# Optimization experiments

Hardware: AMD Instinct MI355X
Metric: run time of the kernel (lower is better)

## Reference

```python
import jax, jax.numpy as jnp
import numpy as np

DIM = 384
HEADS = 12
WIN = (7, 7)
N = WIN[0] * WIN[1]  # 49 tokens per window
B = 2048             # total windows
NW = 64              # windows per image (mask groups)


def _relative_position_index():
    ch, cw = np.meshgrid(np.arange(WIN[0]), np.arange(WIN[1]), indexing='ij')
    coords = np.stack([ch, cw]).reshape(2, -1)                 # [2, N]
    rel = coords[:, :, None] - coords[:, None, :]              # [2, N, N]
    rel = rel.transpose(1, 2, 0)                               # [N, N, 2]
    rel[..., 0] += WIN[0] - 1
    rel[..., 1] += WIN[1] - 1
    rel[..., 0] *= 2 * WIN[1] - 1
    return rel.sum(-1).astype(np.int32)                        # [N, N]


def setup_inputs() -> dict:
    key = jax.random.key(0)
    ks = jax.random.split(key, 7)
    table_sz = (2 * WIN[0] - 1) * (2 * WIN[1] - 1)             # 169
    return {
        'x': jax.random.normal(ks[0], (B, N, DIM), jnp.float32),
        'mask': jax.random.normal(ks[1], (NW, N, N), jnp.float32),
        'qkv_w': jax.random.normal(ks[2], (3 * DIM, DIM), jnp.float32) * (DIM ** -0.5),
        'qkv_b': jnp.zeros((3 * DIM,), jnp.float32),
        'proj_w': jax.random.normal(ks[3], (DIM, DIM), jnp.float32) * (DIM ** -0.5),
        'proj_b': jnp.zeros((DIM,), jnp.float32),
        'rel_table': jax.random.normal(ks[4], (table_sz, HEADS), jnp.float32) * 0.02,
        'rel_index': jnp.asarray(_relative_position_index()),
    }


def reference(x, mask, qkv_w, qkv_b, proj_w, proj_b, rel_table, rel_index):
    b, n, c = x.shape
    h, hd = HEADS, c // HEADS
    scale = hd ** -0.5
    qkv = (x @ qkv_w.T + qkv_b).reshape(b, n, 3, h, hd)
    q, k, v = (qkv[:, :, 0].transpose(0, 2, 1, 3),
               qkv[:, :, 1].transpose(0, 2, 1, 3),
               qkv[:, :, 2].transpose(0, 2, 1, 3))             # [b, h, n, hd]
    attn = jnp.einsum('bhid,bhjd->bhij', q * scale, k)         # [b, h, n, n]
    bias = rel_table[rel_index.reshape(-1)].reshape(n, n, h).transpose(2, 0, 1)
    attn = attn + bias[None]
    nw = mask.shape[0]
    attn = attn.reshape(b // nw, nw, h, n, n) + mask[None, :, None]
    attn = jax.nn.softmax(attn.reshape(b, h, n, n), axis=-1)
    out = jnp.einsum('bhij,bhjd->bihd', attn, v).reshape(b, n, c)
    return out @ proj_w.T + proj_b
```

## Files before the change

kernel.cpp:

```cpp
#include <hip/hip_runtime.h>

#define DIM   384
#define HEADS 12
#define NTOK  49
#define NWIN  2048
#define NMASK 64
#define HD    32
#define MTOT  (NWIN * NTOK)

typedef __bf16 bf16x8 __attribute__((ext_vector_type(8)));
typedef float  floatx4 __attribute__((ext_vector_type(4)));

__device__ __forceinline__ unsigned short f2bf(float f) {
  unsigned int u = __builtin_bit_cast(unsigned int, f);
  u += 0x7fffu + ((u >> 16) & 1u);
  return (unsigned short)(u >> 16);
}
__device__ __forceinline__ void async_copy16(const void* g, void* l) {
  __builtin_amdgcn_global_load_lds((const __attribute__((address_space(1))) void*)g,
                                   (__attribute__((address_space(3))) void*)l, 16, 0, 0);
}

__global__ void prep_kernel(const float* __restrict__ x,
                            const float* __restrict__ qkv_w,
                            const float* __restrict__ proj_w,
                            const float* __restrict__ rel_table,
                            const int*   __restrict__ rel_index,
                            unsigned short* __restrict__ xb,
                            unsigned short* __restrict__ qkv_wb,
                            unsigned short* __restrict__ proj_wb,
                            float* __restrict__ biasP) {
  const int tid  = blockIdx.x * blockDim.x + threadIdx.x;
  const int nthr = gridDim.x * blockDim.x;

  const int nx4 = (MTOT * DIM) / 4;
  for (int i = tid; i < nx4; i += nthr) {
    float4 v = ((const float4*)x)[i];
    ushort4 o = { f2bf(v.x), f2bf(v.y), f2bf(v.z), f2bf(v.w) };
    ((ushort4*)xb)[i] = o;
  }
  const int nw4 = (3 * DIM * DIM) / 4;
  for (int i = tid; i < nw4; i += nthr) {
    float4 v = ((const float4*)qkv_w)[i];
    ushort4 o = { f2bf(v.x), f2bf(v.y), f2bf(v.z), f2bf(v.w) };
    ((ushort4*)qkv_wb)[i] = o;
  }
  const int np4 = (DIM * DIM) / 4;
  for (int i = tid; i < np4; i += nthr) {
    float4 v = ((const float4*)proj_w)[i];
    ushort4 o = { f2bf(v.x), f2bf(v.y), f2bf(v.z), f2bf(v.w) };
    ((ushort4*)proj_wb)[i] = o;
  }
  for (int i = tid; i < 12288; i += nthr) {
    const int lane = i & 63;
    const int t    = (i >> 6) & 15;
    const int h    = i >> 10;
    const int rb   = (t >> 2) * 16 + (lane >> 4) * 4;
    const int c    = (t & 3) * 16 + (lane & 15);
    float4 o;
    float* op = (float*)&o;
#pragma unroll
    for (int reg = 0; reg < 4; reg++) {
      const int r = rb + reg;
      op[reg] = (r < NTOK && c < NTOK)
                  ? rel_table[rel_index[r * NTOK + c] * HEADS + h]
                  : -1e30f;
    }
    ((float4*)biasP)[i] = o;
  }
}

template <int OUT_BF16>
__global__ __launch_bounds__(256, 2)
void gemm_bt(const unsigned short* __restrict__ A,
             const unsigned short* __restrict__ W,
             const float* __restrict__ bias,
             void* __restrict__ Cout,
             int M, int N, int K) {
  constexpr int ESTR = OUT_BF16 ? 144 : 272;
  constexpr int ESZ  = 16 * ESTR;
  __shared__ __align__(16) char lds[OUT_BF16 ? (4 * 2 * 16 * 144)
                                             : (4 * 2 * 16 * 272)];
  char* ldsA = lds;
  char* ldsB = lds + 8192;

  const int tid  = threadIdx.x;
  const int lane = tid & 63;
  const int wave = tid >> 6;
  const int wr   = wave >> 1;
  const int wc   = wave & 1;
  const int q4   = lane >> 4;
  const int lm   = lane & 15;

  const int NT  = N >> 7;
  const int cpx = gridDim.x >> 3;
  const int lin = (blockIdx.x & 7) * cpx + (blockIdx.x >> 3);
  const int tileM = (lin / NT) * 128;
  const int tileN = (lin % NT) * 128;

  const int srow = tid >> 2;
  const int scol = (tid & 3) * 8;
  const unsigned short* gA = A + (size_t)(tileM + srow) * K + scol;
  const unsigned short* gB = W + (size_t)(tileN + srow) * K + scol;
  const int loff = tid * 16;

  const int aoff = (wr * 64 + lm) * 64 + q4 * 16;
  const int boff = (wc * 64 + lm) * 64 + q4 * 16;

  floatx4 acc[4][4] = {};

  for (int k0 = 0; k0 < K; k0 += 32) {
    async_copy16(gA,          ldsA + loff);
    async_copy16(gA + 64 * K, ldsA + 4096 + loff);
    async_copy16(gB,          ldsB + loff);
    async_copy16(gB + 64 * K, ldsB + 4096 + loff);
    gA += 32; gB += 32;
    __syncthreads();

    bf16x8 af[4], bfr[4];
#pragma unroll
    for (int i = 0; i < 4; i++) {
      af[i]  = *(const bf16x8*)(ldsA + aoff + i * 1024);
      bfr[i] = *(const bf16x8*)(ldsB + boff + i * 1024);
    }
#pragma unroll
    for (int i = 0; i < 4; i++)
#pragma unroll
      for (int j = 0; j < 4; j++)
        acc[i][j] = __builtin_amdgcn_mfma_f32_16x16x32_bf16(af[i], bfr[j], acc[i][j], 0, 0, 0);
    __syncthreads();
  }

  float bvj[4];
#pragma unroll
  for (int j = 0; j < 4; j++) bvj[j] = bias[tileN + wc * 64 + j * 16 + lm];

  char* Eb = lds + wave * (2 * ESZ);
#pragma unroll
  for (int i = 0; i < 4; i++) {
    char* Ep = Eb + (i & 1) * ESZ;
    if (OUT_BF16) {
#pragma unroll
      for (int j = 0; j < 4; j++)
#pragma unroll
        for (int r = 0; r < 4; r++)
          *(unsigned short*)(Ep + (q4 * 4 + r) * 144 + (j * 16 + lm) * 2) =
              f2bf(acc[i][j][r] + bvj[j]);
#pragma unroll
      for (int it = 0; it < 2; it++) {
        const int c   = lane + it * 64;
        const int row = c >> 3;
        const int c8  = c & 7;
        const uint4 v = *(const uint4*)(Ep + row * 144 + c8 * 16);
        unsigned short* dst = (unsigned short*)Cout +
            (size_t)(tileM + wr * 64 + i * 16 + row) * N + tileN + wc * 64 + c8 * 8;
        *(uint4*)dst = v;
      }
    } else {
#pragma unroll
      for (int j = 0; j < 4; j++)
#pragma unroll
        for (int r = 0; r < 4; r++)
          *(float*)(Ep + (q4 * 4 + r) * 272 + (j * 16 + lm) * 4) =
              acc[i][j][r] + bvj[j];
#pragma unroll
      for (int it = 0; it < 4; it++) {
        const int c   = lane + it * 64;
        const int row = c >> 4;
        const int c4  = c & 15;
        const uint4 v = *(const uint4*)(Ep + row * 272 + c4 * 16);
        float* dst = (float*)Cout +
            (size_t)(tileM + wr * 64 + i * 16 + row) * N + tileN + wc * 64 + c4 * 4;
        *(uint4*)dst = v;
      }
    }
  }
}

__global__ __launch_bounds__(256)
void attn_mfma(const unsigned short* __restrict__ qkv,
               const float* __restrict__ mask,
               const float* __restrict__ biasP,
               unsigned short* __restrict__ attn_out) {
  __shared__ __align__(16) char lds[4][16128];

  const int tid  = threadIdx.x;
  const int wave = tid >> 6;
  const int lane = tid & 63;
  const int lm   = lane & 15;
  const int q    = lane >> 4;

  const int pair = blockIdx.x * 4 + wave;
  const int b    = pair / HEADS;
  const int h    = pair - b * HEADS;
  const int g    = b & (NMASK - 1);

  char* Wl = lds[wave];
  char* Vt = Wl;
  char* Qb = Wl + 6912;
  char* Kb = Wl + 11008;
  char* Pb = Wl + 6912;

  const unsigned short* qbase = qkv + (size_t)b * NTOK * (3 * DIM) + h * HD;

  const uint4 zero16 = {0u, 0u, 0u, 0u};
#pragma unroll
  for (int r = 0; r < 4; r++) {
    const int row   = r * 16 + (lane >> 2);
    const int chunk = lane & 3;
    uint4 vq = zero16, vk = zero16;
    if (row < NTOK) {
      vq = *(const uint4*)(qbase + (size_t)row * (3 * DIM) + chunk * 8);
      vk = *(const uint4*)(qbase + (size_t)row * (3 * DIM) + DIM + chunk * 8);
    }
    *(uint4*)(Qb + row * 64 + chunk * 16) = vq;
    *(uint4*)(Kb + row * 64 + chunk * 16) = vk;
  }
  const unsigned short* vbase = qbase + 2 * DIM;
#pragma unroll 8
  for (int d = 0; d < HD; d++) {
    unsigned short v = 0;
    if (lane < NTOK) v = vbase[(size_t)lane * (3 * DIM) + d];
    *(unsigned short*)(Vt + d * 144 + lane * 2) = v;
  }
  *(unsigned short*)(Vt + HD * 144 + lane * 2) =
      (lane < NTOK) ? (unsigned short)0x3F80 : (unsigned short)0;

  bf16x8 qf[4], kf[4];
#pragma unroll
  for (int i = 0; i < 4; i++) {
    qf[i] = *(const bf16x8*)(Qb + (i * 16 + lm) * 64 + q * 16);
    kf[i] = *(const bf16x8*)(Kb + (i * 16 + lm) * 64 + q * 16);
  }
  floatx4 S[4][4] = {};
#pragma unroll
  for (int i = 0; i < 4; i++)
#pragma unroll
    for (int j = 0; j < 4; j++)
      S[i][j] = __builtin_amdgcn_mfma_f32_16x16x32_bf16(qf[i], kf[j], S[i][j], 0, 0, 0);

  const float scale = 0.17677669529663687f;
  const float*  bb  = biasP + (size_t)h * 4096;
  const float*  mb  = mask + (size_t)g * (NTOK * NTOK);
#pragma unroll
  for (int i = 0; i < 4; i++) {
#pragma unroll
    for (int j = 0; j < 4; j++) {
      const float4 bm4 = ((const float4*)bb)[(i * 4 + j) * 64 + lane];
      const float* bmp = (const float*)&bm4;
      const int cc = min(j * 16 + lm, NTOK - 1);
#pragma unroll
      for (int r = 0; r < 4; r++) {
        const int rr = min(i * 16 + q * 4 + r, NTOK - 1);
        const float mv = mb[rr * NTOK + cc];
        const float s  = fmaf(S[i][j][r], scale, bmp[r] + mv);
        const float p  = __expf(s);
        *(unsigned short*)(Pb + (i * 16 + q * 4 + r) * 144 + (j * 16 + lm) * 2) = f2bf(p);
      }
    }
  }

  floatx4 O[4][3] = {};
#pragma unroll
  for (int ks = 0; ks < 2; ks++) {
    bf16x8 pf[4], vf[3];
#pragma unroll
    for (int i = 0; i < 4; i++)
      pf[i] = *(const bf16x8*)(Pb + (i * 16 + lm) * 144 + ks * 64 + q * 16);
#pragma unroll
    for (int n = 0; n < 3; n++)
      vf[n] = *(const bf16x8*)(Vt + (n * 16 + lm) * 144 + ks * 64 + q * 16);
#pragma unroll
    for (int i = 0; i < 4; i++)
#pragma unroll
      for (int n = 0; n < 3; n++)
        O[i][n] = __builtin_amdgcn_mfma_f32_16x16x32_bf16(pf[i], vf[n], O[i][n], 0, 0, 0);
  }

  unsigned short* obase = attn_out + (size_t)b * NTOK * DIM + h * HD;
#pragma unroll
  for (int i = 0; i < 4; i++) {
#pragma unroll
    for (int r = 0; r < 4; r++) {
      const float sv  = __shfl(O[i][2][r], tid & 48, 64);
      const float inv = __builtin_amdgcn_rcpf(sv);
      const int row = i * 16 + q * 4 + r;
      if (row < NTOK) {
#pragma unroll
        for (int n = 0; n < 2; n++)
          obase[(size_t)row * DIM + n * 16 + lm] = f2bf(O[i][n][r] * inv);
      }
    }
  }
}

extern "C" void kernel_launch(void* const* d_in, const int* in_sizes, int n_in,
                              void* d_out, int out_size, void* d_ws, size_t ws_size,
                              hipStream_t stream) {
  const float* x         = (const float*)d_in[0];
  const float* mask      = (const float*)d_in[1];
  const float* qkv_w     = (const float*)d_in[2];
  const float* qkv_b     = (const float*)d_in[3];
  const float* proj_w    = (const float*)d_in[4];
  const float* proj_b    = (const float*)d_in[5];
  const float* rel_table = (const float*)d_in[6];
  const int*   rel_index = (const int*)d_in[7];
  float* out = (float*)d_out;

  char* ws = (char*)d_ws;
  unsigned short* xb      = (unsigned short*)(ws);
  unsigned short* qkvbuf  = (unsigned short*)(ws + 77070336);
  unsigned short* qkv_wb  = (unsigned short*)(ws + 308281344);
  unsigned short* proj_wb = (unsigned short*)(ws + 309166080);
  float*          biasP   = (float*)(ws + 309460992);

  prep_kernel<<<2048, 256, 0, stream>>>(x, qkv_w, proj_w, rel_table, rel_index,
                                        xb, qkv_wb, proj_wb, biasP);

  gemm_bt<1><<<dim3((MTOT / 128) * ((3 * DIM) / 128)), 256, 0, stream>>>(
      xb, qkv_wb, qkv_b, qkvbuf, MTOT, 3 * DIM, DIM);

  attn_mfma<<<dim3(NWIN * HEADS / 4), 256, 0, stream>>>(qkvbuf, mask, biasP,
                                                        xb );

  gemm_bt<0><<<dim3((MTOT / 128) * (DIM / 128)), 256, 0, stream>>>(
      xb , proj_wb, proj_b, out, MTOT, DIM, DIM);
}
```

Baseline: 608.9 us.

## Split attention per window-head across four waves and pre-pad mask into MFMA layout

The attention kernel now gives each 256-thread block a single (window, head) pair. Each of the four waves handles one 16-row query tile, sharing Q/K/V staged cooperatively in LDS behind __syncthreads, instead of one wave doing a whole pair alone. V transpose loading is vectorized, and the mask is pre-laid out in the prep kernel into padded MFMA fragment order so the softmax reads coalesced float4s. The block index is also remapped to spread consecutive blocks across the grid. This adds block barriers, 4x more blocks, and extra prep work and workspace for the padded mask.

```diff
diff --git a/kernel.cpp b/kernel.cpp
--- a/kernel.cpp
+++ b/kernel.cpp
@@ -26,10 +26,12 @@
                             const float* __restrict__ proj_w,
                             const float* __restrict__ rel_table,
                             const int*   __restrict__ rel_index,
+                            const float* __restrict__ mask,
                             unsigned short* __restrict__ xb,
                             unsigned short* __restrict__ qkv_wb,
                             unsigned short* __restrict__ proj_wb,
-                            float* __restrict__ biasP) {
+                            float* __restrict__ biasP,
+                            float* __restrict__ maskP) {
   const int tid  = blockIdx.x * blockDim.x + threadIdx.x;
   const int nthr = gridDim.x * blockDim.x;
 
@@ -67,6 +69,23 @@
                   : -1e30f;
     }
     ((float4*)biasP)[i] = o;
+  }
+  for (int i = tid; i < 65536; i += nthr) {
+    const int lane = i & 63;
+    const int t    = (i >> 6) & 15;
+    const int g    = i >> 10;
+    const int rb   = (t >> 2) * 16 + (lane >> 4) * 4;
+    const int c    = (t & 3) * 16 + (lane & 15);
+    float4 o;
+    float* op = (float*)&o;
+#pragma unroll
+    for (int reg = 0; reg < 4; reg++) {
+      const int r = rb + reg;
+      op[reg] = (r < NTOK && c < NTOK)
+                  ? mask[g * (NTOK * NTOK) + r * NTOK + c]
+                  : -1e30f;
+    }
+    ((float4*)maskP)[i] = o;
   }
 }
 
@@ -177,12 +196,16 @@
   }
 }
 
-__global__ __launch_bounds__(256)
+__global__ __launch_bounds__(256, 8)
 void attn_mfma(const unsigned short* __restrict__ qkv,
-               const float* __restrict__ mask,
                const float* __restrict__ biasP,
+               const float* __restrict__ maskP,
                unsigned short* __restrict__ attn_out) {
-  __shared__ __align__(16) char lds[4][16128];
+  __shared__ __align__(16) char lds[16128];
+  char* Vt = lds;
+  char* Qb = lds + 6912;
+  char* Kb = lds + 11008;
+  char* Pb = lds + 6912;
 
   const int tid  = threadIdx.x;
   const int wave = tid >> 6;
@@ -190,25 +213,17 @@
   const int lm   = lane & 15;
   const int q    = lane >> 4;
 
-  const int pair = blockIdx.x * 4 + wave;
+  const int pair = (blockIdx.x & 7) * (NWIN * HEADS / 8) + (blockIdx.x >> 3);
   const int b    = pair / HEADS;
   const int h    = pair - b * HEADS;
   const int g    = b & (NMASK - 1);
 
-  char* Wl = lds[wave];
-  char* Vt = Wl;
-  char* Qb = Wl + 6912;
-  char* Kb = Wl + 11008;
-  char* Pb = Wl + 6912;
-
   const unsigned short* qbase = qkv + (size_t)b * NTOK * (3 * DIM) + h * HD;
 
-  const uint4 zero16 = {0u, 0u, 0u, 0u};
-#pragma unroll
-  for (int r = 0; r < 4; r++) {
-    const int row   = r * 16 + (lane >> 2);
-    const int chunk = lane & 3;
-    uint4 vq = zero16, vk = zero16;
+  {
+    const int row   = tid >> 2;
+    const int chunk = tid & 3;
+    uint4 vq = {0u, 0u, 0u, 0u}, vk = vq;
     if (row < NTOK) {
       vq = *(const uint4*)(qbase + (size_t)row * (3 * DIM) + chunk * 8);
       vk = *(const uint4*)(qbase + (size_t)row * (3 * DIM) + DIM + chunk * 8);
@@ -216,80 +231,72 @@
     *(uint4*)(Qb + row * 64 + chunk * 16) = vq;
     *(uint4*)(Kb + row * 64 + chunk * 16) = vk;
   }
-  const unsigned short* vbase = qbase + 2 * DIM;
-#pragma unroll 8
-  for (int d = 0; d < HD; d++) {
-    unsigned short v = 0;
-    if (lane < NTOK) v = vbase[(size_t)lane * (3 * DIM) + d];
-    *(unsigned short*)(Vt + d * 144 + lane * 2) = v;
-  }
-  *(unsigned short*)(Vt + HD * 144 + lane * 2) =
-      (lane < NTOK) ? (unsigned short)0x3F80 : (unsigned short)0;
-
-  bf16x8 qf[4], kf[4];
-#pragma unroll
-  for (int i = 0; i < 4; i++) {
-    qf[i] = *(const bf16x8*)(Qb + (i * 16 + lm) * 64 + q * 16);
-    kf[i] = *(const bf16x8*)(Kb + (i * 16 + lm) * 64 + q * 16);
-  }
-  floatx4 S[4][4] = {};
-#pragma unroll
-  for (int i = 0; i < 4; i++)
-#pragma unroll
-    for (int j = 0; j < 4; j++)
-      S[i][j] = __builtin_amdgcn_mfma_f32_16x16x32_bf16(qf[i], kf[j], S[i][j], 0, 0, 0);
+  {
+    const int tok = tid >> 2;
+    const int c   = tid & 3;
+    uint4 vv = {0u, 0u, 0u, 0u};
+    if (tok < NTOK) vv = *(const uint4*)(qbase + 2 * DIM + (size_t)tok * (3 * DIM) + c * 8);
+    const unsigned short* e = (const unsigned short*)&vv;
+#pragma unroll
+    for (int j = 0; j < 8; j++)
+      *(unsigned short*)(Vt + (c * 8 + j) * 144 + tok * 2) = e[j];
+    if (tid < 64)
+      *(unsigned short*)(Vt + HD * 144 + tid * 2) =
+          (tid < NTOK) ? (unsigned short)0x3F80 : (unsigned short)0;
+  }
+  __syncthreads();
+
+  bf16x8 qf, kf[4];
+  qf = *(const bf16x8*)(Qb + (wave * 16 + lm) * 64 + q * 16);
+#pragma unroll
+  for (int j = 0; j < 4; j++)
+    kf[j] = *(const bf16x8*)(Kb + (j * 16 + lm) * 64 + q * 16);
+  floatx4 S[4] = {};
+#pragma unroll
+  for (int j = 0; j < 4; j++)
+    S[j] = __builtin_amdgcn_mfma_f32_16x16x32_bf16(qf, kf[j], S[j], 0, 0, 0);
+
+  __syncthreads();
 
   const float scale = 0.17677669529663687f;
-  const float*  bb  = biasP + (size_t)h * 4096;
-  const float*  mb  = mask + (size_t)g * (NTOK * NTOK);
-#pragma unroll
-  for (int i = 0; i < 4; i++) {
-#pragma unroll
-    for (int j = 0; j < 4; j++) {
-      const float4 bm4 = ((const float4*)bb)[(i * 4 + j) * 64 + lane];
-      const float* bmp = (const float*)&bm4;
-      const int cc = min(j * 16 + lm, NTOK - 1);
-#pragma unroll
-      for (int r = 0; r < 4; r++) {
-        const int rr = min(i * 16 + q * 4 + r, NTOK - 1);
-        const float mv = mb[rr * NTOK + cc];
-        const float s  = fmaf(S[i][j][r], scale, bmp[r] + mv);
-        const float p  = __expf(s);
-        *(unsigned short*)(Pb + (i * 16 + q * 4 + r) * 144 + (j * 16 + lm) * 2) = f2bf(p);
-      }
-    }
-  }
-
-  floatx4 O[4][3] = {};
+  const float* bb = biasP + (size_t)h * 4096;
+  const float* mm = maskP + (size_t)g * 4096;
+#pragma unroll
+  for (int j = 0; j < 4; j++) {
+    const int t = wave * 4 + j;
+    const float4 b4 = ((const float4*)bb)[t * 64 + lane];
+    const float4 m4 = ((const float4*)mm)[t * 64 + lane];
+    const float* bp = (const float*)&b4;
+    const float* mp = (const float*)&m4;
+#pragma unroll
+    for (int r = 0; r < 4; r++) {
+      const float s = fmaf(S[j][r], scale, bp[r] + mp[r]);
+      const float p = __expf(s);
+      *(unsigned short*)(Pb + (wave * 16 + q * 4 + r) * 144 + (j * 16 + lm) * 2) = f2bf(p);
+    }
+  }
+
+  floatx4 O[3] = {};
 #pragma unroll
   for (int ks = 0; ks < 2; ks++) {
-    bf16x8 pf[4], vf[3];
-#pragma unroll
-    for (int i = 0; i < 4; i++)
-      pf[i] = *(const bf16x8*)(Pb + (i * 16 + lm) * 144 + ks * 64 + q * 16);
-#pragma unroll
-    for (int n = 0; n < 3; n++)
-      vf[n] = *(const bf16x8*)(Vt + (n * 16 + lm) * 144 + ks * 64 + q * 16);
-#pragma unroll
-    for (int i = 0; i < 4; i++)
-#pragma unroll
-      for (int n = 0; n < 3; n++)
-        O[i][n] = __builtin_amdgcn_mfma_f32_16x16x32_bf16(pf[i], vf[n], O[i][n], 0, 0, 0);
+    const bf16x8 pf = *(const bf16x8*)(Pb + (wave * 16 + lm) * 144 + ks * 64 + q * 16);
+#pragma unroll
+    for (int n = 0; n < 3; n++) {
+      const bf16x8 vf = *(const bf16x8*)(Vt + (n * 16 + lm) * 144 + ks * 64 + q * 16);
+      O[n] = __builtin_amdgcn_mfma_f32_16x16x32_bf16(pf, vf, O[n], 0, 0, 0);
+    }
   }
 
   unsigned short* obase = attn_out + (size_t)b * NTOK * DIM + h * HD;
 #pragma unroll
-  for (int i = 0; i < 4; i++) {
-#pragma unroll
-    for (int r = 0; r < 4; r++) {
-      const float sv  = __shfl(O[i][2][r], tid & 48, 64);
-      const float inv = __builtin_amdgcn_rcpf(sv);
-      const int row = i * 16 + q * 4 + r;
-      if (row < NTOK) {
-#pragma unroll
-        for (int n = 0; n < 2; n++)
-          obase[(size_t)row * DIM + n * 16 + lm] = f2bf(O[i][n][r] * inv);
-      }
+  for (int r = 0; r < 4; r++) {
+    const float sv  = __shfl(O[2][r], lane & 48, 64);
+    const float inv = __builtin_amdgcn_rcpf(sv);
+    const int row = wave * 16 + q * 4 + r;
+    if (row < NTOK) {
+#pragma unroll
+      for (int n = 0; n < 2; n++)
+        obase[(size_t)row * DIM + n * 16 + lm] = f2bf(O[n][r] * inv);
     }
   }
 }
@@ -313,15 +320,16 @@
   unsigned short* qkv_wb  = (unsigned short*)(ws + 308281344);
   unsigned short* proj_wb = (unsigned short*)(ws + 309166080);
   float*          biasP   = (float*)(ws + 309460992);
+  float*          maskP   = (float*)(ws + 309657600);
 
   prep_kernel<<<2048, 256, 0, stream>>>(x, qkv_w, proj_w, rel_table, rel_index,
-                                        xb, qkv_wb, proj_wb, biasP);
+                                        mask, xb, qkv_wb, proj_wb, biasP, maskP);
 
   gemm_bt<1><<<dim3((MTOT / 128) * ((3 * DIM) / 128)), 256, 0, stream>>>(
       xb, qkv_wb, qkv_b, qkvbuf, MTOT, 3 * DIM, DIM);
 
-  attn_mfma<<<dim3(NWIN * HEADS / 4), 256, 0, stream>>>(qkvbuf, mask, biasP,
-                                                        xb );
+  attn_mfma<<<dim3(NWIN * HEADS), 256, 0, stream>>>(qkvbuf, biasP, maskP,
+                                                    xb );
 
   gemm_bt<0><<<dim3((MTOT / 128) * (DIM / 128)), 256, 0, stream>>>(
       xb , proj_wb, proj_b, out, MTOT, DIM, DIM);
```

Measured after the change: 546.4 us. 1.11x faster.
